# Optimization experiments

Hardware: AMD Instinct MI355X
Metric: run time of the kernel (lower is better)

## Reference

```python
import jax, jax.numpy as jnp
import numpy as np

K = 32  # top-k along the feature dim


def setup_inputs() -> dict:
    key = jax.random.key(0)
    B, S, D = 8, 4096, 1024
    x = jax.random.normal(key, (B, S, D), dtype=jnp.float32)
    return {
        "x": x,
        "log_alpha": jnp.zeros((), dtype=jnp.float32),
        "log_sigma": jnp.zeros((), dtype=jnp.float32),
        "ema_mean": jnp.zeros((D,), dtype=jnp.float32),
        "ema_sq": jnp.ones((D,), dtype=jnp.float32),
    }


def reference(x, log_alpha, log_sigma, ema_mean, ema_sq):
    # base = exact (erf) GELU, matching torch.nn.GELU default
    base = jax.nn.gelu(x, approximate=False)
    # per-channel z-score using EMA stats
    ema_var = jnp.clip(ema_sq - ema_mean ** 2, 1e-6, None)
    z_abs = jnp.abs(x - ema_mean) * jax.lax.rsqrt(ema_var)  # [B,S,D]
    # surprise = mean of top-K |z| along feature dim
    top_vals, _ = jax.lax.top_k(z_abs, K)                    # [B,S,K]
    surp = jnp.mean(top_vals, axis=-1, keepdims=True)        # [B,S,1]
    gate = 1.0 + jnp.exp(log_alpha) * jnp.tanh(jnp.exp(log_sigma) * surp)
    return base * gate
```

## Files before the change

### kernel.cpp

```cpp
#include <hip/hip_runtime.h>
#include <math.h>

#define D 1024
#define TOPK 32
#define VPT 16
#define WPB 4

typedef float vfloat4 __attribute__((ext_vector_type(4)));

__device__ __forceinline__ float waveMax(float v) {
#pragma unroll
  for (int off = 32; off >= 1; off >>= 1)
    v = fmaxf(v, __shfl_xor(v, off, 64));
  return v;
}
__device__ __forceinline__ float waveSumF(float v) {
#pragma unroll
  for (int off = 32; off >= 1; off >>= 1)
    v += __shfl_xor(v, off, 64);
  return v;
}

__device__ __forceinline__ float fast_gelu(float x) {
  const float x2 = x * x;
  const float p = __builtin_fmaf(0.044715f, x2, 1.0f);
  const float a = -1.5957691216f * x * p;
  const float e = __expf(a);
  const float r = __builtin_amdgcn_rcpf(1.0f + e);
  return x * r;
}

__global__ __launch_bounds__(256) void prep_stats(const float* __restrict__ ema_mean,
                                                  const float* __restrict__ ema_sq,
                                                  float* __restrict__ inv_std) {
  int i = blockIdx.x * 256 + threadIdx.x;
  if (i < D) {
    float m = ema_mean[i];
    float v = ema_sq[i] - m * m;
    inv_std[i] = rsqrtf(fmaxf(v, 1e-6f));
  }
}

__global__ __launch_bounds__(256, 4) void gelu_gate(const float* __restrict__ x,
                                                    const float* __restrict__ p_la,
                                                    const float* __restrict__ p_ls,
                                                    const float* __restrict__ ema_mean,
                                                    const float* __restrict__ inv_std,
                                                    float* __restrict__ out,
                                                    int n_rows) {
  const int wave = threadIdx.x >> 6;
  const int lane = threadIdx.x & 63;
  const int row = blockIdx.x * WPB + wave;
  if (row >= n_rows) return;
  const float* __restrict__ xr = x + (size_t)row * D;
  float* __restrict__ orow = out + (size_t)row * D;

  float xv[VPT], za[VPT];
#pragma unroll
  for (int j = 0; j < 4; ++j) {
    const int c = j * 256 + lane * 4;
    const float4 xx = *reinterpret_cast<const float4*>(xr + c);
    const float4 mm = *reinterpret_cast<const float4*>(ema_mean + c);
    const float4 ss = *reinterpret_cast<const float4*>(inv_std + c);
    xv[4 * j + 0] = xx.x; xv[4 * j + 1] = xx.y;
    xv[4 * j + 2] = xx.z; xv[4 * j + 3] = xx.w;
    za[4 * j + 0] = fabsf(xx.x - mm.x) * ss.x;
    za[4 * j + 1] = fabsf(xx.y - mm.y) * ss.y;
    za[4 * j + 2] = fabsf(xx.z - mm.z) * ss.z;
    za[4 * j + 3] = fabsf(xx.w - mm.w) * ss.w;
  }

  float m = 0.0f;
#pragma unroll
  for (int i = 0; i < VPT; ++i) m = fmaxf(m, za[i]);
  m = waveMax(m);

  float lo = 0.0f;
  float hi = __uint_as_float(__float_as_uint(m) + 1u);
  for (;;) {
    const float mid = 0.5f * (lo + hi);
    if (!(mid > lo) || !(mid < hi)) break;
    int c = 0;
#pragma unroll
    for (int i = 0; i < VPT; ++i)
      c += (int)__popcll(__ballot(za[i] >= mid));
    if (c >= TOPK) {
      lo = mid;
      if (c == TOPK) break;
    } else {
      hi = mid;
    }
  }
  const float t = lo;

  float s = 0.0f;
  int cg = 0;
#pragma unroll
  for (int i = 0; i < VPT; ++i) {
    const bool g = za[i] > t;
    s += g ? za[i] : 0.0f;
    cg += (int)__popcll(__ballot(g));
  }
  s = waveSumF(s);
  const float topsum = s + (float)(TOPK - cg) * t;
  const float surp = topsum * (1.0f / (float)TOPK);
  const float gate = 1.0f + expf(p_la[0]) * tanhf(expf(p_ls[0]) * surp);

#pragma unroll
  for (int j = 0; j < 4; ++j) {
    const int c = j * 256 + lane * 4;
    vfloat4 o;
    o.x = fast_gelu(xv[4 * j + 0]) * gate;
    o.y = fast_gelu(xv[4 * j + 1]) * gate;
    o.z = fast_gelu(xv[4 * j + 2]) * gate;
    o.w = fast_gelu(xv[4 * j + 3]) * gate;
    __builtin_nontemporal_store(o, reinterpret_cast<vfloat4*>(orow + c));
  }
}

extern "C" void kernel_launch(void* const* d_in, const int* in_sizes, int n_in,
                              void* d_out, int out_size, void* d_ws, size_t ws_size,
                              hipStream_t stream) {
  const float* x    = (const float*)d_in[0];
  const float* la   = (const float*)d_in[1];
  const float* ls   = (const float*)d_in[2];
  const float* mean = (const float*)d_in[3];
  const float* sq   = (const float*)d_in[4];
  float* out = (float*)d_out;
  float* inv_std = (float*)d_ws;

  const int n = in_sizes[0];
  const int n_rows = n / D;

  prep_stats<<<(D + 255) / 256, 256, 0, stream>>>(mean, sq, inv_std);

  const int grid = (n_rows + WPB - 1) / WPB;
  gelu_gate<<<grid, WPB * 64, 0, stream>>>(x, la, ls, mean, inv_std, out, n_rows);
}
```

Measured before the change: 239.8 us.

## Process two rows per wave with interleaved bisection and precomputed GELU

After: 242.9 us. No clear change (+1.3%).

```diff
diff --git a/kernel.cpp b/kernel.cpp
--- a/kernel.cpp
+++ b/kernel.cpp
@@ -4,21 +4,24 @@
 #define D 1024
 #define TOPK 32
 #define VPT 16
-#define WPB 4
+#define RPW 2
+#define WAVES 4
 
 typedef float vfloat4 __attribute__((ext_vector_type(4)));
 
-__device__ __forceinline__ float waveMax(float v) {
+__device__ __forceinline__ void waveMax2(float& a, float& b) {
 #pragma unroll
-  for (int off = 32; off >= 1; off >>= 1)
-    v = fmaxf(v, __shfl_xor(v, off, 64));
-  return v;
+  for (int off = 32; off >= 1; off >>= 1) {
+    a = fmaxf(a, __shfl_xor(a, off, 64));
+    b = fmaxf(b, __shfl_xor(b, off, 64));
+  }
 }
-__device__ __forceinline__ float waveSumF(float v) {
+__device__ __forceinline__ void waveSum2(float& a, float& b) {
 #pragma unroll
-  for (int off = 32; off >= 1; off >>= 1)
-    v += __shfl_xor(v, off, 64);
-  return v;
+  for (int off = 32; off >= 1; off >>= 1) {
+    a += __shfl_xor(a, off, 64);
+    b += __shfl_xor(b, off, 64);
+  }
 }
 
 __device__ __forceinline__ float fast_gelu(float x) {
@@ -26,95 +29,143 @@
   const float p = __builtin_fmaf(0.044715f, x2, 1.0f);
   const float a = -1.5957691216f * x * p;
   const float e = __expf(a);
-  const float r = __builtin_amdgcn_rcpf(1.0f + e);
-  return x * r;
+  return x * __builtin_amdgcn_rcpf(1.0f + e);
+}
+__device__ __forceinline__ float fast_tanh_pos(float y) {
+  const float e = __expf(2.0f * y);
+  return 1.0f - 2.0f * __builtin_amdgcn_rcpf(e + 1.0f);
 }
 
 __global__ __launch_bounds__(256) void prep_stats(const float* __restrict__ ema_mean,
                                                   const float* __restrict__ ema_sq,
-                                                  float* __restrict__ inv_std) {
+                                                  const float* __restrict__ p_la,
+                                                  const float* __restrict__ p_ls,
+                                                  float* __restrict__ ws) {
   int i = blockIdx.x * 256 + threadIdx.x;
   if (i < D) {
     float m = ema_mean[i];
     float v = ema_sq[i] - m * m;
-    inv_std[i] = rsqrtf(fmaxf(v, 1e-6f));
+    ws[i] = rsqrtf(fmaxf(v, 1e-6f));
+  }
+  if (i == 0) {
+    ws[D] = expf(p_la[0]);
+    ws[D + 1] = expf(p_ls[0]);
   }
 }
 
 __global__ __launch_bounds__(256, 4) void gelu_gate(const float* __restrict__ x,
-                                                    const float* __restrict__ p_la,
-                                                    const float* __restrict__ p_ls,
                                                     const float* __restrict__ ema_mean,
-                                                    const float* __restrict__ inv_std,
+                                                    const float* __restrict__ ws,
                                                     float* __restrict__ out,
                                                     int n_rows) {
   const int wave = threadIdx.x >> 6;
   const int lane = threadIdx.x & 63;
-  const int row = blockIdx.x * WPB + wave;
-  if (row >= n_rows) return;
-  const float* __restrict__ xr = x + (size_t)row * D;
-  float* __restrict__ orow = out + (size_t)row * D;
+  const int w = blockIdx.x * WAVES + wave;
+  const int row0 = w * RPW;
+  if (row0 >= n_rows) return;
+  const bool has1 = (row0 + 1) < n_rows;
+  const float* __restrict__ xr0 = x + (size_t)row0 * D;
+  const float* __restrict__ xr1 = x + (size_t)(has1 ? row0 + 1 : row0) * D;
 
-  float xv[VPT], za[VPT];
+  float za0[VPT], za1[VPT], g0[VPT], g1[VPT];
 #pragma unroll
   for (int j = 0; j < 4; ++j) {
     const int c = j * 256 + lane * 4;
-    const float4 xx = *reinterpret_cast<const float4*>(xr + c);
+    const float4 a0 = *reinterpret_cast<const float4*>(xr0 + c);
+    const float4 a1 = *reinterpret_cast<const float4*>(xr1 + c);
     const float4 mm = *reinterpret_cast<const float4*>(ema_mean + c);
-    const float4 ss = *reinterpret_cast<const float4*>(inv_std + c);
-    xv[4 * j + 0] = xx.x; xv[4 * j + 1] = xx.y;
-    xv[4 * j + 2] = xx.z; xv[4 * j + 3] = xx.w;
-    za[4 * j + 0] = fabsf(xx.x - mm.x) * ss.x;
-    za[4 * j + 1] = fabsf(xx.y - mm.y) * ss.y;
-    za[4 * j + 2] = fabsf(xx.z - mm.z) * ss.z;
-    za[4 * j + 3] = fabsf(xx.w - mm.w) * ss.w;
+    const float4 ss = *reinterpret_cast<const float4*>(ws + c);
+    const float xs0[4] = {a0.x, a0.y, a0.z, a0.w};
+    const float xs1[4] = {a1.x, a1.y, a1.z, a1.w};
+    const float ms[4] = {mm.x, mm.y, mm.z, mm.w};
+    const float is[4] = {ss.x, ss.y, ss.z, ss.w};
+#pragma unroll
+    for (int q = 0; q < 4; ++q) {
+      const int i = 4 * j + q;
+      za0[i] = fabsf(xs0[q] - ms[q]) * is[q];
+      za1[i] = fabsf(xs1[q] - ms[q]) * is[q];
+      g0[i] = fast_gelu(xs0[q]);
+      g1[i] = fast_gelu(xs1[q]);
+    }
   }
 
-  float m = 0.0f;
+  float m0 = 0.0f, m1 = 0.0f;
 #pragma unroll
-  for (int i = 0; i < VPT; ++i) m = fmaxf(m, za[i]);
-  m = waveMax(m);
+  for (int i = 0; i < VPT; ++i) {
+    m0 = fmaxf(m0, za0[i]);
+    m1 = fmaxf(m1, za1[i]);
+  }
+  waveMax2(m0, m1);
 
-  float lo = 0.0f;
-  float hi = __uint_as_float(__float_as_uint(m) + 1u);
-  for (;;) {
-    const float mid = 0.5f * (lo + hi);
-    if (!(mid > lo) || !(mid < hi)) break;
-    int c = 0;
+  float lo0 = 0.0f, hi0 = __uint_as_float(__float_as_uint(m0) + 1u);
+  float lo1 = 0.0f, hi1 = __uint_as_float(__float_as_uint(m1) + 1u);
+  bool done0 = false, done1 = !has1;
+  while (!done0 || !done1) {
+    float mid0 = 0.5f * (lo0 + hi0);
+    float mid1 = 0.5f * (lo1 + hi1);
+    if (!done0 && (!(mid0 > lo0) || !(mid0 < hi0))) done0 = true;
+    if (!done1 && (!(mid1 > lo1) || !(mid1 < hi1))) done1 = true;
+    if (done0) mid0 = lo0;
+    if (done1) mid1 = lo1;
+    if (done0 && done1) break;
+    int c0 = 0, c1 = 0;
 #pragma unroll
-    for (int i = 0; i < VPT; ++i)
-      c += (int)__popcll(__ballot(za[i] >= mid));
-    if (c >= TOPK) {
-      lo = mid;
-      if (c == TOPK) break;
-    } else {
-      hi = mid;
+    for (int i = 0; i < VPT; ++i) {
+      c0 += (int)__popcll(__ballot(za0[i] >= mid0));
+      c1 += (int)__popcll(__ballot(za1[i] >= mid1));
+    }
+    if (!done0) {
+      if (c0 >= TOPK) { lo0 = mid0; if (c0 == TOPK) done0 = true; }
+      else hi0 = mid0;
+    }
+    if (!done1) {
+      if (c1 >= TOPK) { lo1 = mid1; if (c1 == TOPK) done1 = true; }
+      else hi1 = mid1;
     }
   }
-  const float t = lo;
+  const float t0 = lo0, t1 = lo1;
 
-  float s = 0.0f;
-  int cg = 0;
+  float s0 = 0.0f, s1 = 0.0f;
+  int cg0 = 0, cg1 = 0;
 #pragma unroll
   for (int i = 0; i < VPT; ++i) {
-    const bool g = za[i] > t;
-    s += g ? za[i] : 0.0f;
-    cg += (int)__popcll(__ballot(g));
+    const bool b0 = za0[i] > t0;
+    const bool b1 = za1[i] > t1;
+    s0 += b0 ? za0[i] : 0.0f;
+    s1 += b1 ? za1[i] : 0.0f;
+    cg0 += (int)__popcll(__ballot(b0));
+    cg1 += (int)__popcll(__ballot(b1));
   }
-  s = waveSumF(s);
-  const float topsum = s + (float)(TOPK - cg) * t;
-  const float surp = topsum * (1.0f / (float)TOPK);
-  const float gate = 1.0f + expf(p_la[0]) * tanhf(expf(p_ls[0]) * surp);
+  waveSum2(s0, s1);
+  const float ea = ws[D], es = ws[D + 1];
+  const float surp0 = (s0 + (float)(TOPK - cg0) * t0) * (1.0f / (float)TOPK);
+  const float surp1 = (s1 + (float)(TOPK - cg1) * t1) * (1.0f / (float)TOPK);
+  const float gate0 = 1.0f + ea * fast_tanh_pos(es * surp0);
+  const float gate1 = 1.0f + ea * fast_tanh_pos(es * surp1);
 
+  float* __restrict__ o0 = out + (size_t)row0 * D;
 #pragma unroll
   for (int j = 0; j < 4; ++j) {
     const int c = j * 256 + lane * 4;
     vfloat4 o;
-    o.x = fast_gelu(xv[4 * j + 0]) * gate;
-    o.y = fast_gelu(xv[4 * j + 1]) * gate;
-    o.z = fast_gelu(xv[4 * j + 2]) * gate;
-    o.w = fast_gelu(xv[4 * j + 3]) * gate;
-    __builtin_nontemporal_store(o, reinterpret_cast<vfloat4*>(orow + c));
+    o.x = g0[4 * j + 0] * gate0;
+    o.y = g0[4 * j + 1] * gate0;
+    o.z = g0[4 * j + 2] * gate0;
+    o.w = g0[4 * j + 3] * gate0;
+    __builtin_nontemporal_store(o, reinterpret_cast<vfloat4*>(o0 + c));
+  }
+  if (has1) {
+    float* __restrict__ o1 = out + (size_t)(row0 + 1) * D;
+#pragma unroll
+    for (int j = 0; j < 4; ++j) {
+      const int c = j * 256 + lane * 4;
+      vfloat4 o;
+      o.x = g1[4 * j + 0] * gate1;
+      o.y = g1[4 * j + 1] * gate1;
+      o.z = g1[4 * j + 2] * gate1;
+      o.w = g1[4 * j + 3] * gate1;
+      __builtin_nontemporal_store(o, reinterpret_cast<vfloat4*>(o1 + c));
+    }
   }
 }
 
@@ -127,13 +178,14 @@
   const float* mean = (const float*)d_in[3];
   const float* sq   = (const float*)d_in[4];
   float* out = (float*)d_out;
-  float* inv_std = (float*)d_ws;
+  float* ws = (float*)d_ws;
 
   const int n = in_sizes[0];
   const int n_rows = n / D;
 
-  prep_stats<<<(D + 255) / 256, 256, 0, stream>>>(mean, sq, inv_std);
+  prep_stats<<<(D + 255) / 256, 256, 0, stream>>>(mean, sq, la, ls, ws);
 
-  const int grid = (n_rows + WPB - 1) / WPB;
-  gelu_gate<<<grid, WPB * 64, 0, stream>>>(x, la, ls, mean, inv_std, out, n_rows);
+  const int rows_per_block = RPW * WAVES;
+  const int grid = (n_rows + rows_per_block - 1) / rows_per_block;
+  gelu_gate<<<grid, WAVES * 64, 0, stream>>>(x, mean, ws, out, n_rows);
 }
```

## Split into gate and apply kernels with bracketed, tolerance-limited top-k threshold search

Applied to the files above, without the earlier changes.

Measured after the change: 252.6 us. +5.4%, slower.

```diff
diff --git a/kernel.cpp b/kernel.cpp
--- a/kernel.cpp
+++ b/kernel.cpp
@@ -4,92 +4,94 @@
 #define D 1024
 #define TOPK 32
 #define VPT 16
-#define WPB 4
+#define EPS 0.0625f
 
 typedef float vfloat4 __attribute__((ext_vector_type(4)));
 
-__device__ __forceinline__ float waveMax(float v) {
-#pragma unroll
-  for (int off = 32; off >= 1; off >>= 1)
-    v = fmaxf(v, __shfl_xor(v, off, 64));
-  return v;
-}
 __device__ __forceinline__ float waveSumF(float v) {
 #pragma unroll
-  for (int off = 32; off >= 1; off >>= 1)
-    v += __shfl_xor(v, off, 64);
+  for (int off = 32; off >= 1; off >>= 1) v += __shfl_xor(v, off, 64);
   return v;
 }
 
 __device__ __forceinline__ float fast_gelu(float x) {
   const float x2 = x * x;
   const float p = __builtin_fmaf(0.044715f, x2, 1.0f);
-  const float a = -1.5957691216f * x * p;
-  const float e = __expf(a);
-  const float r = __builtin_amdgcn_rcpf(1.0f + e);
-  return x * r;
+  const float e = __expf(-1.5957691216f * x * p);
+  return x * __builtin_amdgcn_rcpf(1.0f + e);
+}
+__device__ __forceinline__ float fast_tanh_pos(float y) {
+  const float e = __expf(2.0f * y);
+  return 1.0f - 2.0f * __builtin_amdgcn_rcpf(e + 1.0f);
+}
+
+__device__ __forceinline__ int countGE(const float* za, float t) {
+  int c = 0;
+#pragma unroll
+  for (int i = 0; i < VPT; ++i) c += (int)__popcll(__ballot(za[i] >= t));
+  return c;
 }
 
 __global__ __launch_bounds__(256) void prep_stats(const float* __restrict__ ema_mean,
                                                   const float* __restrict__ ema_sq,
-                                                  float* __restrict__ inv_std) {
+                                                  const float* __restrict__ p_la,
+                                                  const float* __restrict__ p_ls,
+                                                  float* __restrict__ ws) {
   int i = blockIdx.x * 256 + threadIdx.x;
   if (i < D) {
     float m = ema_mean[i];
     float v = ema_sq[i] - m * m;
-    inv_std[i] = rsqrtf(fmaxf(v, 1e-6f));
+    ws[i] = rsqrtf(fmaxf(v, 1e-6f));
+  }
+  if (i == 0) {
+    ws[D] = expf(p_la[0]);
+    ws[D + 1] = expf(p_ls[0]);
   }
 }
 
-__global__ __launch_bounds__(256, 4) void gelu_gate(const float* __restrict__ x,
-                                                    const float* __restrict__ p_la,
-                                                    const float* __restrict__ p_ls,
-                                                    const float* __restrict__ ema_mean,
-                                                    const float* __restrict__ inv_std,
-                                                    float* __restrict__ out,
-                                                    int n_rows) {
+__global__ __launch_bounds__(256) void row_gate(const float* __restrict__ x,
+                                                const float* __restrict__ ema_mean,
+                                                const float* __restrict__ ws,
+                                                float* __restrict__ gates,
+                                                int n_rows) {
   const int wave = threadIdx.x >> 6;
   const int lane = threadIdx.x & 63;
-  const int row = blockIdx.x * WPB + wave;
+  const int row = blockIdx.x * 4 + wave;
   if (row >= n_rows) return;
   const float* __restrict__ xr = x + (size_t)row * D;
-  float* __restrict__ orow = out + (size_t)row * D;
 
-  float xv[VPT], za[VPT];
+  float za[VPT];
 #pragma unroll
   for (int j = 0; j < 4; ++j) {
-    const int c = j * 256 + lane * 4;
-    const float4 xx = *reinterpret_cast<const float4*>(xr + c);
-    const float4 mm = *reinterpret_cast<const float4*>(ema_mean + c);
-    const float4 ss = *reinterpret_cast<const float4*>(inv_std + c);
-    xv[4 * j + 0] = xx.x; xv[4 * j + 1] = xx.y;
-    xv[4 * j + 2] = xx.z; xv[4 * j + 3] = xx.w;
+    const int ch = j * 256 + lane * 4;
+    const float4 xx = *reinterpret_cast<const float4*>(xr + ch);
+    const float4 mm = *reinterpret_cast<const float4*>(ema_mean + ch);
+    const float4 ss = *reinterpret_cast<const float4*>(ws + ch);
     za[4 * j + 0] = fabsf(xx.x - mm.x) * ss.x;
     za[4 * j + 1] = fabsf(xx.y - mm.y) * ss.y;
     za[4 * j + 2] = fabsf(xx.z - mm.z) * ss.z;
     za[4 * j + 3] = fabsf(xx.w - mm.w) * ss.w;
   }
 
-  float m = 0.0f;
-#pragma unroll
-  for (int i = 0; i < VPT; ++i) m = fmaxf(m, za[i]);
-  m = waveMax(m);
-
-  float lo = 0.0f;
-  float hi = __uint_as_float(__float_as_uint(m) + 1u);
-  for (;;) {
+  float lo = 0.0f, hi = 3.6f;
+  int cl = D;
+  {
+    const int cp = countGE(za, 1.2f);
+    if (cp >= TOPK) { lo = 1.2f; cl = cp; }
+  }
+  {
+    int chi = countGE(za, hi);
+    while (chi >= TOPK) {
+      lo = hi; cl = chi;
+      hi *= 2.0f;
+      chi = countGE(za, hi);
+    }
+  }
+  while (cl != TOPK && (hi - lo) > EPS) {
     const float mid = 0.5f * (lo + hi);
-    if (!(mid > lo) || !(mid < hi)) break;
-    int c = 0;
-#pragma unroll
-    for (int i = 0; i < VPT; ++i)
-      c += (int)__popcll(__ballot(za[i] >= mid));
-    if (c >= TOPK) {
-      lo = mid;
-      if (c == TOPK) break;
-    } else {
-      hi = mid;
-    }
+    const int cm = countGE(za, mid);
+    if (cm >= TOPK) { lo = mid; cl = cm; }
+    else hi = mid;
   }
   const float t = lo;
 
@@ -102,19 +104,25 @@
     cg += (int)__popcll(__ballot(g));
   }
   s = waveSumF(s);
-  const float topsum = s + (float)(TOPK - cg) * t;
-  const float surp = topsum * (1.0f / (float)TOPK);
-  const float gate = 1.0f + expf(p_la[0]) * tanhf(expf(p_ls[0]) * surp);
+  const float surp = (s + (float)(TOPK - cg) * t) * (1.0f / (float)TOPK);
+  const float gate = 1.0f + ws[D] * fast_tanh_pos(ws[D + 1] * surp);
+  if (lane == 0) gates[row] = gate;
+}
 
-#pragma unroll
-  for (int j = 0; j < 4; ++j) {
-    const int c = j * 256 + lane * 4;
+__global__ __launch_bounds__(256) void apply_gate(const float* __restrict__ x,
+                                                  const float* __restrict__ gates,
+                                                  float* __restrict__ out,
+                                                  int n_rows) {
+  for (int row = blockIdx.x; row < n_rows; row += gridDim.x) {
+    const float gate = gates[row];
+    const size_t base = (size_t)row * D + threadIdx.x * 4;
+    const float4 v = *reinterpret_cast<const float4*>(x + base);
     vfloat4 o;
-    o.x = fast_gelu(xv[4 * j + 0]) * gate;
-    o.y = fast_gelu(xv[4 * j + 1]) * gate;
-    o.z = fast_gelu(xv[4 * j + 2]) * gate;
-    o.w = fast_gelu(xv[4 * j + 3]) * gate;
-    __builtin_nontemporal_store(o, reinterpret_cast<vfloat4*>(orow + c));
+    o.x = fast_gelu(v.x) * gate;
+    o.y = fast_gelu(v.y) * gate;
+    o.z = fast_gelu(v.z) * gate;
+    o.w = fast_gelu(v.w) * gate;
+    __builtin_nontemporal_store(o, reinterpret_cast<vfloat4*>(out + base));
   }
 }
 
@@ -127,13 +135,16 @@
   const float* mean = (const float*)d_in[3];
   const float* sq   = (const float*)d_in[4];
   float* out = (float*)d_out;
-  float* inv_std = (float*)d_ws;
+  float* ws = (float*)d_ws;
+  float* gates = ws + 2048;
 
   const int n = in_sizes[0];
   const int n_rows = n / D;
 
-  prep_stats<<<(D + 255) / 256, 256, 0, stream>>>(mean, sq, inv_std);
+  prep_stats<<<(D + 255) / 256, 256, 0, stream>>>(mean, sq, la, ls, ws);
 
-  const int grid = (n_rows + WPB - 1) / WPB;
-  gelu_gate<<<grid, WPB * 64, 0, stream>>>(x, la, ls, mean, inv_std, out, n_rows);
+  row_gate<<<(n_rows + 3) / 4, 256, 0, stream>>>(x, mean, ws, gates, n_rows);
+
+  const int gridB = 8192;
+  apply_gate<<<gridB, 256, 0, stream>>>(x, gates, out, n_rows);
 }
```
